# Performance work log

Hardware: AMD Instinct MI355X
Metric: run time of the kernel (lower is better)

## Reference

```python
import jax, jax.numpy as jnp
import numpy as np

N_NODES = 50000
N_EDGES = 800000
EMB = 128
HID = [128, 128]
OUT = 64
CE = 8  # stand-in for CROSS_ENTROPY_INDEXES: first 8 output columns get sigmoid


def _linear_params(key, d_in, d_out):
    k1, k2 = jax.random.split(key)
    s = 1.0 / np.sqrt(d_in)
    w = jax.random.uniform(k1, (d_in, d_out), minval=-s, maxval=s, dtype=jnp.float32)
    b = jax.random.uniform(k2, (d_out,), minval=-s, maxval=s, dtype=jnp.float32)
    return w, b


def setup_inputs() -> dict:
    key = jax.random.key(0)
    ks = jax.random.split(key, 16)
    z = jax.random.normal(ks[0], (N_NODES, EMB), dtype=jnp.float32)
    edge_index = jax.random.randint(ks[1], (2, N_EDGES), 0, N_NODES, dtype=jnp.int64)
    # SAGEConv params: neighbor weight (with bias) + root weight
    w1_n, b1 = _linear_params(ks[2], EMB, HID[0])
    w1_r, _ = _linear_params(ks[3], EMB, HID[0])
    w2_n, b2 = _linear_params(ks[4], HID[0], HID[1])
    w2_r, _ = _linear_params(ks[5], HID[0], HID[1])
    wf_n, bf = _linear_params(ks[6], HID[1], OUT)
    wf_r, _ = _linear_params(ks[7], HID[1], OUT)
    # initial residual linears: emb -> hid[1], emb -> out
    w_res1, b_res1 = _linear_params(ks[8], EMB, HID[1])
    w_res2, b_res2 = _linear_params(ks[9], EMB, OUT)
    return dict(z=z, edge_index=edge_index,
                w1_n=w1_n, w1_r=w1_r, b1=b1,
                w2_n=w2_n, w2_r=w2_r, b2=b2,
                wf_n=wf_n, wf_r=wf_r, bf=bf,
                w_res1=w_res1, b_res1=b_res1,
                w_res2=w_res2, b_res2=b_res2)


def _sage(x, src, dst, w_n, w_r, b, n_nodes):
    # mean-aggregate neighbor features at target nodes, then affine combine with root
    msg = x[src]                                        # [E, d]
    agg = jax.ops.segment_sum(msg, dst, num_segments=n_nodes)
    deg = jax.ops.segment_sum(jnp.ones_like(dst, dtype=x.dtype), dst, num_segments=n_nodes)
    mean = agg / jnp.maximum(deg, 1.0)[:, None]
    return mean @ w_n + x @ w_r + b


def reference(z, edge_index, w1_n, w1_r, b1, w2_n, w2_r, b2, wf_n, wf_r, bf,
              w_res1, b_res1, w_res2, b_res2):
    n = z.shape[0]
    src, dst = edge_index[0], edge_index[1]
    h = jax.nn.relu(_sage(z, src, dst, w1_n, w1_r, b1, n))
    # mid layer (dropout is identity in eval) + initial residual
    h = jax.nn.relu(_sage(h, src, dst, w2_n, w2_r, b2, n))
    h = h + (z @ w_res1 + b_res1)
    # final conv + final residual
    h = _sage(h, src, dst, wf_n, wf_r, bf, n)
    h = h + (z @ w_res2 + b_res2)
    # sigmoid on cross-entropy columns
    h = h.at[:, :CE].set(jax.nn.sigmoid(h[:, :CE]))
    return h
```

## Files before the change

### kernel.cpp

```cpp
#include <hip/hip_runtime.h>
#include <hip/hip_bf16.h>
#include <math.h>

#define NN 50000
#define NE 800000
#define NB 391
#define EPB 6250

typedef short bf16x8 __attribute__((ext_vector_type(8)));
typedef float f32x4 __attribute__((ext_vector_type(4)));
typedef unsigned short us4 __attribute__((ext_vector_type(4)));
typedef unsigned short us8 __attribute__((ext_vector_type(8)));
typedef unsigned int u32x4 __attribute__((ext_vector_type(4)));

__device__ __forceinline__ float bf2f(unsigned short u) {
  union { unsigned int i; float f; } x; x.i = ((unsigned int)u) << 16; return x.f;
}
__device__ __forceinline__ unsigned short f2bf(float f) {
  union { float f; unsigned int i; } x; x.f = f;
  unsigned int i = x.i;
  unsigned int r = i + 0x7FFF + ((i >> 16) & 1);
  return (unsigned short)(r >> 16);
}
__device__ __forceinline__ unsigned long long pk64(f32x4 v) {
  union { us4 s; unsigned long long u; } x;
  x.s[0] = f2bf(v[0]); x.s[1] = f2bf(v[1]); x.s[2] = f2bf(v[2]); x.s[3] = f2bf(v[3]);
  return x.u;
}
__device__ __forceinline__ us4 pack4(f32x4 v) {
  us4 o; o[0] = f2bf(v[0]); o[1] = f2bf(v[1]); o[2] = f2bf(v[2]); o[3] = f2bf(v[3]);
  return o;
}

__global__ __launch_bounds__(512) void bscan_kernel(const int* __restrict__ bhist,
                                                    int* __restrict__ bucket_off,
                                                    int* __restrict__ gcur) {
  __shared__ int s[512];
  int t = threadIdx.x;
  int v = (t < NB) ? bhist[t] : 0;
  s[t] = v; __syncthreads();
  for (int off = 1; off < 512; off <<= 1) {
    int x = (t >= off) ? s[t - off] : 0;
    __syncthreads();
    s[t] += x;
    __syncthreads();
  }
  if (t < NB) { bucket_off[t] = s[t] - v; gcur[t] = 0; }
  if (t == NB - 1) bucket_off[NB] = s[t];
}

__global__ __launch_bounds__(256) void bscat_kernel(const int* __restrict__ srcn,
                                                    const int* __restrict__ dstn,
                                                    const int* __restrict__ bucket_off,
                                                    int* __restrict__ gcur,
                                                    unsigned long long* __restrict__ ebuf) {
  __shared__ int hist[NB];
  __shared__ int base[NB];
  for (int i = threadIdx.x; i < NB; i += 256) hist[i] = 0;
  __syncthreads();
  int e0 = blockIdx.x * EPB;
  for (int i = threadIdx.x; i < EPB; i += 256)
    atomicAdd(&hist[dstn[e0 + i] >> 7], 1);
  __syncthreads();
  for (int i = threadIdx.x; i < NB; i += 256) {
    int c = hist[i];
    base[i] = c ? (bucket_off[i] + atomicAdd(&gcur[i], c)) : 0;
  }
  __syncthreads();
  for (int i = threadIdx.x; i < EPB; i += 256) {
    int s = srcn[e0 + i], d = dstn[e0 + i];
    int b = d >> 7;
    int pos = atomicSub(&hist[b], 1) - 1;
    ebuf[(size_t)base[b] + pos] = ((unsigned long long)(unsigned)d << 32) | (unsigned)s;
  }
}

__global__ __launch_bounds__(256) void bfill_kernel(const unsigned long long* __restrict__ ebuf,
                                                    const int* __restrict__ bucket_off,
                                                    int* __restrict__ rowoff,
                                                    int* __restrict__ csr) {
  int b = blockIdx.x;
  int bo = bucket_off[b], cnt = bucket_off[b + 1] - bo;
  __shared__ int ndeg[128], noff[128];
  int t = threadIdx.x;
  if (t < 128) ndeg[t] = 0;
  __syncthreads();
  for (int i = t; i < cnt; i += 256)
    atomicAdd(&ndeg[(int)(ebuf[bo + i] >> 32) & 127], 1);
  __syncthreads();
  if (t < 128) noff[t] = ndeg[t];
  __syncthreads();
  for (int off = 1; off < 128; off <<= 1) {
    int x = 0;
    if (t < 128 && t >= off) x = noff[t - off];
    __syncthreads();
    if (t < 128 && t >= off) noff[t] += x;
    __syncthreads();
  }
  if (t < 128) {
    int ex = noff[t] - ndeg[t];
    noff[t] = ex;
    int node = b * 128 + t;
    if (node < NN) rowoff[node] = bo + ex;
  }
  if (b == NB - 1 && t == 0) rowoff[NN] = NE;
  __syncthreads();
  for (int i = t; i < cnt; i += 256) {
    unsigned long long e = ebuf[bo + i];
    int dl = (int)(e >> 32) & 127;
    int pos = atomicSub(&ndeg[dl], 1) - 1;
    csr[bo + noff[dl] + pos] = (int)(unsigned)e;
  }
}

__global__ __launch_bounds__(256) void setup_kernel(
    const float* __restrict__ z, unsigned short* __restrict__ A1,
    const float* __restrict__ w1n, const float* __restrict__ w1r,
    const float* __restrict__ w2n, const float* __restrict__ w2r,
    const float* __restrict__ wfn, const float* __restrict__ wfr,
    const float* __restrict__ wr1, const float* __restrict__ wr2,
    unsigned short* __restrict__ Bp1, unsigned short* __restrict__ Bp2,
    unsigned short* __restrict__ Bp3,
    const int* __restrict__ dstn, int* __restrict__ bhist) {
  __shared__ int h[NB];
  int b = blockIdx.x;
  if (b < 6250) {
    int i = b * 256 + threadIdx.x;
    if (i >= NN * 128 / 4) return;
    int i4 = i * 4;
    int row = i4 >> 7, c = i4 & 127;
    f32x4 v = *(const f32x4*)(z + i4);
    us4 o = { f2bf(v[0]), f2bf(v[1]), f2bf(v[2]), f2bf(v[3]) };
    *(us4*)(A1 + (size_t)row * 256 + 128 + c) = o;
  } else if (b < 6314) {
    int g = (b - 6250) * 256 + threadIdx.x;
    unsigned short* D; int NT, fi;
    int which;
    if      (g < 10240) { fi = g;         D = Bp1; NT = 20; which = 1; }
    else if (g < 14336) { fi = g - 10240; D = Bp2; NT = 8;  which = 2; }
    else if (g < 16384) { fi = g - 14336; D = Bp3; NT = 4;  which = 3; }
    else return;
    int lane = fi & 63, t = fi >> 6;
    int nt = t % NT, k0i = t / NT;
    int m = lane & 15, q = lane >> 4;
    int kb = k0i * 32 + q * 8;
    int n = nt * 16 + m;
    int hi = (kb >= 128);
    int k0_ = kb - (hi ? 128 : 0);
    const float* W = nullptr; int Nseg = 128; int nn = n;
    if (which == 1) {
      if (n < 128)      { W = hi ? w1r : w1n; nn = n; Nseg = 128; }
      else if (n < 256) { W = hi ? wr1 : nullptr; nn = n - 128; Nseg = 128; }
      else              { W = hi ? wr2 : nullptr; nn = n - 256; Nseg = 64; }
    } else if (which == 2) { W = hi ? w2r : w2n; Nseg = 128; }
    else                   { W = hi ? wfr : wfn; Nseg = 64; }
    unsigned short o[8];
#pragma unroll
    for (int j = 0; j < 8; j++)
      o[j] = W ? f2bf(W[(size_t)(k0_ + j) * Nseg + nn]) : (unsigned short)0;
    *(us8*)(D + (size_t)fi * 8) = *(const us8*)o;
  } else {
    for (int i = threadIdx.x; i < NB; i += 256) h[i] = 0;
    __syncthreads();
    int e0 = (b - 6314) * EPB;
    for (int i = threadIdx.x; i < EPB; i += 256)
      atomicAdd(&h[dstn[e0 + i] >> 7], 1);
    __syncthreads();
    for (int i = threadIdx.x; i < NB; i += 256)
      if (h[i]) atomicAdd(&bhist[i], h[i]);
  }
}

__global__ __launch_bounds__(256) void agg_kernel(const unsigned short* __restrict__ feat, int fstride,
                                                  unsigned short* __restrict__ outm, int ostride,
                                                  const int* __restrict__ rowoff,
                                                  const int* __restrict__ csr) {
  int wave = threadIdx.x >> 6, lane = threadIdx.x & 63;
  int node = blockIdx.x * 4 + wave;
  if (node >= NN) return;
  int beg = rowoff[node], end = rowoff[node + 1];
  int g = lane >> 4;
  int c = (lane & 15) << 3;
  float a[8];
#pragma unroll
  for (int i = 0; i < 8; i++) a[i] = 0.f;
  int e1 = end - 1;
  for (int j = beg + g; j < end; j += 16) {
    int j1 = (j + 4 < e1) ? j + 4 : e1;
    int j2 = (j + 8 < e1) ? j + 8 : e1;
    int j3 = (j + 12 < e1) ? j + 12 : e1;
    int s0 = csr[j], s1 = csr[j1], s2 = csr[j2], s3 = csr[j3];
    float w1 = (j + 4 < end) ? 1.f : 0.f;
    float w2 = (j + 8 < end) ? 1.f : 0.f;
    float w3 = (j + 12 < end) ? 1.f : 0.f;
    u32x4 v0 = *(const u32x4*)(feat + (size_t)s0 * fstride + c);
    u32x4 v1 = *(const u32x4*)(feat + (size_t)s1 * fstride + c);
    u32x4 v2 = *(const u32x4*)(feat + (size_t)s2 * fstride + c);
    u32x4 v3 = *(const u32x4*)(feat + (size_t)s3 * fstride + c);
#pragma unroll
    for (int i = 0; i < 4; i++) {
      float l0 = bf2f((unsigned short)(v0[i] & 0xffff));
      float h0 = bf2f((unsigned short)(v0[i] >> 16));
      l0 = fmaf(w1, bf2f((unsigned short)(v1[i] & 0xffff)), l0);
      h0 = fmaf(w1, bf2f((unsigned short)(v1[i] >> 16)), h0);
      l0 = fmaf(w2, bf2f((unsigned short)(v2[i] & 0xffff)), l0);
      h0 = fmaf(w2, bf2f((unsigned short)(v2[i] >> 16)), h0);
      l0 = fmaf(w3, bf2f((unsigned short)(v3[i] & 0xffff)), l0);
      h0 = fmaf(w3, bf2f((unsigned short)(v3[i] >> 16)), h0);
      a[2*i] += l0;
      a[2*i+1] += h0;
    }
  }
#pragma unroll
  for (int i = 0; i < 8; i++) {
    a[i] += __shfl_xor(a[i], 16, 64);
    a[i] += __shfl_xor(a[i], 32, 64);
  }
  if (g == 0) {
    float inv = 1.f / fmaxf((float)(end - beg), 1.f);
    unsigned int o[4];
#pragma unroll
    for (int i = 0; i < 4; i++)
      o[i] = ((unsigned int)f2bf(a[2*i+1] * inv) << 16) | f2bf(a[2*i] * inv);
    *(u32x4*)(outm + (size_t)node * ostride + c) = *(const u32x4*)o;
  }
}

__global__ __launch_bounds__(256) void gemm1_kernel(
    const unsigned short* __restrict__ A,
    const unsigned short* __restrict__ Bp,
    const float* __restrict__ b1, const float* __restrict__ br1, const float* __restrict__ br2,
    unsigned short* __restrict__ h1out,
    unsigned short* __restrict__ res1, unsigned short* __restrict__ res2)
{
  const int NT = 20, TILES = 4;
  __shared__ unsigned short Bs[TILES * 8 * 512];
  int tid = threadIdx.x;
  int wave = tid >> 6, lane = tid & 63;
  int xg = blockIdx.x;
  int ybase = xg * TILES;
  int row0 = blockIdx.y * 128 + wave * 16;
  int m = lane & 15, q = lane >> 4;
  const float* bias; unsigned short* dst; int dstride, cbb; int relu;
  if (xg < 2)      { bias = b1 + xg * 64;        dst = h1out; dstride = 256; cbb = xg * 64;        relu = 1; }
  else if (xg < 4) { bias = br1 + (xg - 2) * 64; dst = res1;  dstride = 128; cbb = (xg - 2) * 64;  relu = 0; }
  else             { bias = br2;                 dst = res2;  dstride = 64;  cbb = 0;              relu = 0; }

  const unsigned short* arow0 = A + (size_t)(row0 + m) * 256 + q * 8;
  const unsigned short* arow1 = arow0 + 64 * 256;
  bf16x8 af0[8], af1[8];
#pragma unroll
  for (int k0i = 0; k0i < 8; ++k0i) {
    af0[k0i] = *(const bf16x8*)(arow0 + k0i * 32);
    af1[k0i] = *(const bf16x8*)(arow1 + k0i * 32);
  }
#pragma unroll
  for (int i = tid; i < TILES * 64 * 8; i += 256) {
    int k0i = i / (TILES * 64), r = i % (TILES * 64);
    *(us8*)(Bs + (size_t)k0i * TILES * 512 + (size_t)r * 8) =
        *(const us8*)(Bp + ((size_t)k0i * NT + ybase) * 512 + (size_t)r * 8);
  }
  __syncthreads();
  f32x4 acc[2][TILES];
#pragma unroll
  for (int h = 0; h < 2; h++)
#pragma unroll
    for (int i = 0; i < TILES; i++) acc[h][i] = (f32x4){0.f, 0.f, 0.f, 0.f};
#pragma unroll
  for (int k0i = 0; k0i < 8; ++k0i) {
    const unsigned short* bk = Bs + (size_t)k0i * TILES * 512 + lane * 8;
#pragma unroll
    for (int s = 0; s < TILES; ++s) {
      bf16x8 bfr = *(const bf16x8*)(bk + s * 512);
      acc[0][s] = __builtin_amdgcn_mfma_f32_16x16x32_bf16(bfr, af0[k0i], acc[0][s], 0, 0, 0);
      acc[1][s] = __builtin_amdgcn_mfma_f32_16x16x32_bf16(bfr, af1[k0i], acc[1][s], 0, 0, 0);
    }
  }
  int src0 = m + ((q & 1) ? 32 : 0);
#pragma unroll
  for (int h = 0; h < 2; h++) {
    int row = row0 + h * 64 + m;
#pragma unroll
    for (int p = 0; p < 2; p++) {
      f32x4 v0 = acc[h][2 * p], v1 = acc[h][2 * p + 1];
      f32x4 bb0 = *(const f32x4*)(bias + 32 * p + 4 * q);
      f32x4 bb1 = *(const f32x4*)(bias + 32 * p + 16 + 4 * q);
#pragma unroll
      for (int r = 0; r < 4; r++) { v0[r] += bb0[r]; v1[r] += bb1[r]; }
      if (relu) {
#pragma unroll
        for (int r = 0; r < 4; r++) { v0[r] = fmaxf(v0[r], 0.f); v1[r] = fmaxf(v1[r], 0.f); }
      }
      unsigned long long d0 = pk64(v0), d1 = pk64(v1);
      unsigned long long a0 = __shfl(d0, src0, 64);
      unsigned long long b0 = __shfl(d0, src0 + 16, 64);
      unsigned long long a1 = __shfl(d1, src0, 64);
      unsigned long long b1v = __shfl(d1, src0 + 16, 64);
      unsigned long long lo = (q >> 1) ? a1 : a0;
      unsigned long long hi = (q >> 1) ? b1v : b0;
      if (row < NN) {
        unsigned long long ov[2] = { lo, hi };
        *(us8*)(dst + (size_t)row * dstride + cbb + 32 * p + 8 * q) = *(const us8*)ov;
      }
    }
  }
}

__global__ __launch_bounds__(256) void gemm2_kernel(
    const unsigned short* __restrict__ A,
    const unsigned short* __restrict__ Bp,
    const float* __restrict__ b2,
    const unsigned short* __restrict__ res1,
    unsigned short* __restrict__ out_bf)
{
  const int NT = 8, TILES = 4;
  __shared__ unsigned short Bs[TILES * 8 * 512];
  int tid = threadIdx.x;
  int wave = tid >> 6, lane = tid & 63;
  int xg = blockIdx.x;
  int ybase = xg * TILES;
  int cbb = xg * 64;
  const float* bias = b2 + cbb;
  int row0 = blockIdx.y * 128 + wave * 16;
  int m = lane & 15, q = lane >> 4;
  const unsigned short* arow0 = A + (size_t)(row0 + m) * 256 + q * 8;
  const unsigned short* arow1 = arow0 + 64 * 256;
  bf16x8 af0[8], af1[8];
#pragma unroll
  for (int k0i = 0; k0i < 8; ++k0i) {
    af0[k0i] = *(const bf16x8*)(arow0 + k0i * 32);
    af1[k0i] = *(const bf16x8*)(arow1 + k0i * 32);
  }
#pragma unroll
  for (int i = tid; i < TILES * 64 * 8; i += 256) {
    int k0i = i / (TILES * 64), r = i % (TILES * 64);
    *(us8*)(Bs + (size_t)k0i * TILES * 512 + (size_t)r * 8) =
        *(const us8*)(Bp + ((size_t)k0i * NT + ybase) * 512 + (size_t)r * 8);
  }
  __syncthreads();
  f32x4 acc[2][TILES];
#pragma unroll
  for (int h = 0; h < 2; h++)
#pragma unroll
    for (int i = 0; i < TILES; i++) acc[h][i] = (f32x4){0.f, 0.f, 0.f, 0.f};
#pragma unroll
  for (int k0i = 0; k0i < 8; ++k0i) {
    const unsigned short* bk = Bs + (size_t)k0i * TILES * 512 + lane * 8;
#pragma unroll
    for (int s = 0; s < TILES; ++s) {
      bf16x8 bfr = *(const bf16x8*)(bk + s * 512);
      acc[0][s] = __builtin_amdgcn_mfma_f32_16x16x32_bf16(bfr, af0[k0i], acc[0][s], 0, 0, 0);
      acc[1][s] = __builtin_amdgcn_mfma_f32_16x16x32_bf16(bfr, af1[k0i], acc[1][s], 0, 0, 0);
    }
  }
  int src0 = m + ((q & 1) ? 32 : 0);
#pragma unroll
  for (int h = 0; h < 2; h++) {
    int row = row0 + h * 64 + m;
#pragma unroll
    for (int p = 0; p < 2; p++) {
      f32x4 v0 = acc[h][2 * p], v1 = acc[h][2 * p + 1];
      f32x4 bb0 = *(const f32x4*)(bias + 32 * p + 4 * q);
      f32x4 bb1 = *(const f32x4*)(bias + 32 * p + 16 + 4 * q);
#pragma unroll
      for (int r = 0; r < 4; r++) {
        v0[r] = fmaxf(v0[r] + bb0[r], 0.f);
        v1[r] = fmaxf(v1[r] + bb1[r], 0.f);
      }
      unsigned long long d0 = pk64(v0), d1 = pk64(v1);
      unsigned long long a0 = __shfl(d0, src0, 64);
      unsigned long long b0 = __shfl(d0, src0 + 16, 64);
      unsigned long long a1 = __shfl(d1, src0, 64);
      unsigned long long b1v = __shfl(d1, src0 + 16, 64);
      unsigned long long lo = (q >> 1) ? a1 : a0;
      unsigned long long hi = (q >> 1) ? b1v : b0;
      if (row < NN) {
        size_t off = cbb + 32 * p + 8 * q;
        us8 rv = *(const us8*)(res1 + (size_t)row * 128 + off);
        unsigned long long ov[2] = { lo, hi };
        unsigned short* e = (unsigned short*)ov;
#pragma unroll
        for (int r = 0; r < 8; r++) e[r] = f2bf(bf2f(e[r]) + bf2f(rv[r]));
        *(us8*)(out_bf + (size_t)row * 256 + off) = *(const us8*)ov;
      }
    }
  }
}

__global__ __launch_bounds__(256) void gemm3_kernel(
    const unsigned short* __restrict__ A,
    const unsigned short* __restrict__ Bp,
    const float* __restrict__ bias,
    const unsigned short* __restrict__ res2,
    float* __restrict__ out_f)
{
  const int NT = 4, TILES = 4;
  __shared__ unsigned short Bs[TILES * 8 * 512];
  int tid = threadIdx.x;
  int wave = tid >> 6, lane = tid & 63;
  int row0 = blockIdx.y * 64 + wave * 16;
  int m = lane & 15, q = lane >> 4;
  const unsigned short* arow = A + (size_t)(row0 + m) * 256 + q * 8;
  bf16x8 af[8];
#pragma unroll
  for (int k0i = 0; k0i < 8; ++k0i) af[k0i] = *(const bf16x8*)(arow + k0i * 32);
#pragma unroll
  for (int i = tid; i < TILES * 64 * 8; i += 256) {
    int k0i = i / (TILES * 64), r = i % (TILES * 64);
    *(us8*)(Bs + (size_t)k0i * TILES * 512 + (size_t)r * 8) =
        *(const us8*)(Bp + ((size_t)k0i * NT) * 512 + (size_t)r * 8);
  }
  __syncthreads();
  f32x4 acc[TILES];
#pragma unroll
  for (int i = 0; i < TILES; i++) acc[i] = (f32x4){0.f, 0.f, 0.f, 0.f};
#pragma unroll
  for (int k0i = 0; k0i < 8; ++k0i) {
    const unsigned short* bk = Bs + (size_t)k0i * TILES * 512 + lane * 8;
#pragma unroll
    for (int s = 0; s < TILES; ++s) {
      bf16x8 bfr = *(const bf16x8*)(bk + s * 512);
      acc[s] = __builtin_amdgcn_mfma_f32_16x16x32_bf16(bfr, af[k0i], acc[s], 0, 0, 0);
    }
  }
  int row = row0 + m;
  if (row >= NN) return;
  int cb = q * 4;
#pragma unroll
  for (int s = 0; s < TILES; ++s) {
    int col = s * 16 + cb;
    f32x4 v = acc[s];
    f32x4 bb = *(const f32x4*)(bias + col);
    us4 rv = *(const us4*)(res2 + (size_t)row * 64 + col);
#pragma unroll
    for (int r = 0; r < 4; r++) v[r] += bb[r] + bf2f(rv[r]);
    if (col < 8) {
#pragma unroll
      for (int r = 0; r < 4; r++) v[r] = 1.f / (1.f + __expf(-v[r]));
    }
    *(f32x4*)(out_f + (size_t)row * 64 + col) = v;
  }
}

extern "C" void kernel_launch(void* const* d_in, const int* in_sizes, int n_in,
                              void* d_out, int out_size, void* d_ws, size_t ws_size,
                              hipStream_t stream) {
  const float* z   = (const float*)d_in[0];
  const int*   edge = (const int*)d_in[1];
  const int*   srcn = edge;
  const int*   dstn = edge + NE;
  const float* w1n = (const float*)d_in[2];
  const float* w1r = (const float*)d_in[3];
  const float* b1  = (const float*)d_in[4];
  const float* w2n = (const float*)d_in[5];
  const float* w2r = (const float*)d_in[6];
  const float* b2  = (const float*)d_in[7];
  const float* wfn = (const float*)d_in[8];
  const float* wfr = (const float*)d_in[9];
  const float* bfb = (const float*)d_in[10];
  const float* wr1 = (const float*)d_in[11];
  const float* br1 = (const float*)d_in[12];
  const float* wr2 = (const float*)d_in[13];
  const float* br2 = (const float*)d_in[14];
  float* out = (float*)d_out;

  char* p = (char*)d_ws;
  auto alloc = [&](size_t bytes) { char* r = p; p += (bytes + 255) & ~255ull; return r; };
  int* rowoff = (int*)alloc((size_t)(NN + 1) * 4);
  int* bhist  = (int*)alloc((size_t)NB * 4);
  int* bucket_off = (int*)alloc((size_t)(NB + 1) * 4);
  int* gcur   = (int*)alloc((size_t)NB * 4);
  int* csr    = (int*)alloc((size_t)NE * 4);
  unsigned short* A1 = (unsigned short*)alloc((size_t)NN * 256 * 2);
  unsigned short* A2 = (unsigned short*)alloc((size_t)NN * 256 * 2);
  unsigned short* res1 = (unsigned short*)alloc((size_t)NN * 128 * 2);
  unsigned short* res2 = (unsigned short*)alloc((size_t)NN * 64 * 2);
  unsigned short* Bp1 = (unsigned short*)alloc(10240 * 8 * 2);
  unsigned short* Bp2 = (unsigned short*)alloc(4096 * 8 * 2);
  unsigned short* Bp3 = (unsigned short*)alloc(2048 * 8 * 2);
  unsigned short* A3 = A1;
  unsigned long long* ebuf = (unsigned long long*)res1;

  hipMemsetAsync(bhist, 0, (size_t)NB * 4, stream);
  setup_kernel<<<6442, 256, 0, stream>>>(z, A1, w1n, w1r, w2n, w2r, wfn, wfr, wr1, wr2,
                                         Bp1, Bp2, Bp3, dstn, bhist);
  bscan_kernel<<<1, 512, 0, stream>>>(bhist, bucket_off, gcur);
  bscat_kernel<<<128, 256, 0, stream>>>(srcn, dstn, bucket_off, gcur, ebuf);
  bfill_kernel<<<NB, 256, 0, stream>>>(ebuf, bucket_off, rowoff, csr);

  const int gy128 = (NN + 127) / 128;
  const int gy64  = (NN + 63) / 64;
  const int agg_blocks = (NN + 3) / 4;

  agg_kernel<<<agg_blocks, 256, 0, stream>>>(A1 + 128, 256, A1, 256, rowoff, csr);
  gemm1_kernel<<<dim3(5, gy128), 256, 0, stream>>>(A1, Bp1, b1, br1, br2, A2 + 128, res1, res2);

  agg_kernel<<<agg_blocks, 256, 0, stream>>>(A2 + 128, 256, A2, 256, rowoff, csr);
  gemm2_kernel<<<dim3(2, gy128), 256, 0, stream>>>(A2, Bp2, b2, res1, A3 + 128);

  agg_kernel<<<agg_blocks, 256, 0, stream>>>(A3 + 128, 256, A3, 256, rowoff, csr);
  gemm3_kernel<<<dim3(1, gy64), 256, 0, stream>>>(A3, Bp3, bfb, res2, out);
}
```

Measured before the change: 284.9 us.

## Fuse neighbor aggregation into per-layer GEMM kernels and merge bucket scan

Each SAGE layer's mean aggregation now runs inside its GEMM kernel: 512-thread blocks gather neighbor means for 128 rows into swizzled shared memory, then run MFMA against B tiles streamed per K-slice. This removes the intermediate mean buffer round-trip and three kernel launches. The standalone bucket-scan kernel is dropped; scatter and fill kernels recompute the prefix scan from the histogram, and feature buffers shrink to a 128-wide padded layout. The cost is only 391 blocks per layer, each with long serial gather loops, extra barriers per K-step, and redundant scans in every scatter/fill block.

```diff
diff --git a/kernel.cpp b/kernel.cpp
--- a/kernel.cpp
+++ b/kernel.cpp
@@ -3,6 +3,7 @@
 #include <math.h>
 
 #define NN 50000
+#define NNP 50048
 #define NE 800000
 #define NB 391
 #define EPB 6250
@@ -27,17 +28,9 @@
   x.s[0] = f2bf(v[0]); x.s[1] = f2bf(v[1]); x.s[2] = f2bf(v[2]); x.s[3] = f2bf(v[3]);
   return x.u;
 }
-__device__ __forceinline__ us4 pack4(f32x4 v) {
-  us4 o; o[0] = f2bf(v[0]); o[1] = f2bf(v[1]); o[2] = f2bf(v[2]); o[3] = f2bf(v[3]);
-  return o;
-}
-
-__global__ __launch_bounds__(512) void bscan_kernel(const int* __restrict__ bhist,
-                                                    int* __restrict__ bucket_off,
-                                                    int* __restrict__ gcur) {
-  __shared__ int s[512];
+
+__device__ __forceinline__ int scan_incl_512(int v, int* s) {
   int t = threadIdx.x;
-  int v = (t < NB) ? bhist[t] : 0;
   s[t] = v; __syncthreads();
   for (int off = 1; off < 512; off <<= 1) {
     int x = (t >= off) ? s[t - off] : 0;
@@ -45,29 +38,33 @@
     s[t] += x;
     __syncthreads();
   }
-  if (t < NB) { bucket_off[t] = s[t] - v; gcur[t] = 0; }
-  if (t == NB - 1) bucket_off[NB] = s[t];
-}
-
-__global__ __launch_bounds__(256) void bscat_kernel(const int* __restrict__ srcn,
+  return s[t];
+}
+
+__global__ __launch_bounds__(512) void bscat_kernel(const int* __restrict__ srcn,
                                                     const int* __restrict__ dstn,
-                                                    const int* __restrict__ bucket_off,
+                                                    const int* __restrict__ bhist,
                                                     int* __restrict__ gcur,
                                                     unsigned long long* __restrict__ ebuf) {
+  __shared__ int sbuf[512];
+  __shared__ int boff[NB];
   __shared__ int hist[NB];
   __shared__ int base[NB];
-  for (int i = threadIdx.x; i < NB; i += 256) hist[i] = 0;
+  int t = threadIdx.x;
+  int v = (t < NB) ? bhist[t] : 0;
+  int incl = scan_incl_512(v, sbuf);
+  if (t < NB) { boff[t] = incl - v; hist[t] = 0; }
   __syncthreads();
   int e0 = blockIdx.x * EPB;
-  for (int i = threadIdx.x; i < EPB; i += 256)
+  for (int i = t; i < EPB; i += 512)
     atomicAdd(&hist[dstn[e0 + i] >> 7], 1);
   __syncthreads();
-  for (int i = threadIdx.x; i < NB; i += 256) {
+  for (int i = t; i < NB; i += 512) {
     int c = hist[i];
-    base[i] = c ? (bucket_off[i] + atomicAdd(&gcur[i], c)) : 0;
-  }
-  __syncthreads();
-  for (int i = threadIdx.x; i < EPB; i += 256) {
+    base[i] = c ? (boff[i] + atomicAdd(&gcur[i], c)) : 0;
+  }
+  __syncthreads();
+  for (int i = t; i < EPB; i += 512) {
     int s = srcn[e0 + i], d = dstn[e0 + i];
     int b = d >> 7;
     int pos = atomicSub(&hist[b], 1) - 1;
@@ -75,17 +72,22 @@
   }
 }
 
-__global__ __launch_bounds__(256) void bfill_kernel(const unsigned long long* __restrict__ ebuf,
-                                                    const int* __restrict__ bucket_off,
+__global__ __launch_bounds__(512) void bfill_kernel(const unsigned long long* __restrict__ ebuf,
+                                                    const int* __restrict__ bhist,
                                                     int* __restrict__ rowoff,
                                                     int* __restrict__ csr) {
+  __shared__ int sbuf[512];
+  __shared__ int sb[2];
+  __shared__ int ndeg[128], noff[128];
   int b = blockIdx.x;
-  int bo = bucket_off[b], cnt = bucket_off[b + 1] - bo;
-  __shared__ int ndeg[128], noff[128];
   int t = threadIdx.x;
+  int v = (t < NB) ? bhist[t] : 0;
+  int incl = scan_incl_512(v, sbuf);
+  if (t == b) { sb[0] = incl - v; sb[1] = v; }
   if (t < 128) ndeg[t] = 0;
   __syncthreads();
-  for (int i = t; i < cnt; i += 256)
+  int bo = sb[0], cnt = sb[1];
+  for (int i = t; i < cnt; i += 512)
     atomicAdd(&ndeg[(int)(ebuf[bo + i] >> 32) & 127], 1);
   __syncthreads();
   if (t < 128) noff[t] = ndeg[t];
@@ -105,7 +107,7 @@
   }
   if (b == NB - 1 && t == 0) rowoff[NN] = NE;
   __syncthreads();
-  for (int i = t; i < cnt; i += 256) {
+  for (int i = t; i < cnt; i += 512) {
     unsigned long long e = ebuf[bo + i];
     int dl = (int)(e >> 32) & 127;
     int pos = atomicSub(&ndeg[dl], 1) - 1;
@@ -114,7 +116,7 @@
 }
 
 __global__ __launch_bounds__(256) void setup_kernel(
-    const float* __restrict__ z, unsigned short* __restrict__ A1,
+    const float* __restrict__ z, unsigned short* __restrict__ Z16,
     const float* __restrict__ w1n, const float* __restrict__ w1r,
     const float* __restrict__ w2n, const float* __restrict__ w2r,
     const float* __restrict__ wfn, const float* __restrict__ wfr,
@@ -131,7 +133,7 @@
     int row = i4 >> 7, c = i4 & 127;
     f32x4 v = *(const f32x4*)(z + i4);
     us4 o = { f2bf(v[0]), f2bf(v[1]), f2bf(v[2]), f2bf(v[3]) };
-    *(us4*)(A1 + (size_t)row * 256 + 128 + c) = o;
+    *(us4*)(Z16 + (size_t)row * 128 + c) = o;
   } else if (b < 6314) {
     int g = (b - 6250) * 256 + threadIdx.x;
     unsigned short* D; int NT, fi;
@@ -171,272 +173,280 @@
   }
 }
 
-__global__ __launch_bounds__(256) void agg_kernel(const unsigned short* __restrict__ feat, int fstride,
-                                                  unsigned short* __restrict__ outm, int ostride,
-                                                  const int* __restrict__ rowoff,
-                                                  const int* __restrict__ csr) {
-  int wave = threadIdx.x >> 6, lane = threadIdx.x & 63;
-  int node = blockIdx.x * 4 + wave;
-  if (node >= NN) return;
-  int beg = rowoff[node], end = rowoff[node + 1];
+__device__ __forceinline__ void gather_mean(const unsigned short* __restrict__ feat,
+                                            int row0,
+                                            const int* __restrict__ rowoff,
+                                            const int* __restrict__ csr,
+                                            unsigned short* meanS) {
+  int tid = threadIdx.x;
+  int w = tid >> 6, lane = tid & 63;
   int g = lane >> 4;
   int c = (lane & 15) << 3;
-  float a[8];
-#pragma unroll
-  for (int i = 0; i < 8; i++) a[i] = 0.f;
-  int e1 = end - 1;
-  for (int j = beg + g; j < end; j += 16) {
-    int j1 = (j + 4 < e1) ? j + 4 : e1;
-    int j2 = (j + 8 < e1) ? j + 8 : e1;
-    int j3 = (j + 12 < e1) ? j + 12 : e1;
-    int s0 = csr[j], s1 = csr[j1], s2 = csr[j2], s3 = csr[j3];
-    float w1 = (j + 4 < end) ? 1.f : 0.f;
-    float w2 = (j + 8 < end) ? 1.f : 0.f;
-    float w3 = (j + 12 < end) ? 1.f : 0.f;
-    u32x4 v0 = *(const u32x4*)(feat + (size_t)s0 * fstride + c);
-    u32x4 v1 = *(const u32x4*)(feat + (size_t)s1 * fstride + c);
-    u32x4 v2 = *(const u32x4*)(feat + (size_t)s2 * fstride + c);
-    u32x4 v3 = *(const u32x4*)(feat + (size_t)s3 * fstride + c);
-#pragma unroll
-    for (int i = 0; i < 4; i++) {
-      float l0 = bf2f((unsigned short)(v0[i] & 0xffff));
-      float h0 = bf2f((unsigned short)(v0[i] >> 16));
-      l0 = fmaf(w1, bf2f((unsigned short)(v1[i] & 0xffff)), l0);
-      h0 = fmaf(w1, bf2f((unsigned short)(v1[i] >> 16)), h0);
-      l0 = fmaf(w2, bf2f((unsigned short)(v2[i] & 0xffff)), l0);
-      h0 = fmaf(w2, bf2f((unsigned short)(v2[i] >> 16)), h0);
-      l0 = fmaf(w3, bf2f((unsigned short)(v3[i] & 0xffff)), l0);
-      h0 = fmaf(w3, bf2f((unsigned short)(v3[i] >> 16)), h0);
-      a[2*i] += l0;
-      a[2*i+1] += h0;
-    }
-  }
-#pragma unroll
-  for (int i = 0; i < 8; i++) {
-    a[i] += __shfl_xor(a[i], 16, 64);
-    a[i] += __shfl_xor(a[i], 32, 64);
-  }
-  if (g == 0) {
-    float inv = 1.f / fmaxf((float)(end - beg), 1.f);
-    unsigned int o[4];
-#pragma unroll
-    for (int i = 0; i < 4; i++)
-      o[i] = ((unsigned int)f2bf(a[2*i+1] * inv) << 16) | f2bf(a[2*i] * inv);
-    *(u32x4*)(outm + (size_t)node * ostride + c) = *(const u32x4*)o;
-  }
-}
-
-__global__ __launch_bounds__(256) void gemm1_kernel(
-    const unsigned short* __restrict__ A,
+#pragma unroll 2
+  for (int i = 0; i < 16; ++i) {
+    int node = row0 + w * 16 + i;
+    int beg = 0, end = 0;
+    if (node < NN) { beg = rowoff[node]; end = rowoff[node + 1]; }
+    float a[8];
+#pragma unroll
+    for (int k = 0; k < 8; ++k) a[k] = 0.f;
+    int e1 = end - 1;
+    for (int j = beg + g; j < end; j += 16) {
+      int j1 = (j + 4 < e1) ? j + 4 : e1;
+      int j2 = (j + 8 < e1) ? j + 8 : e1;
+      int j3 = (j + 12 < e1) ? j + 12 : e1;
+      int s0 = csr[j], s1 = csr[j1], s2 = csr[j2], s3 = csr[j3];
+      float w1 = (j + 4 < end) ? 1.f : 0.f;
+      float w2 = (j + 8 < end) ? 1.f : 0.f;
+      float w3 = (j + 12 < end) ? 1.f : 0.f;
+      u32x4 v0 = *(const u32x4*)(feat + (size_t)s0 * 128 + c);
+      u32x4 v1 = *(const u32x4*)(feat + (size_t)s1 * 128 + c);
+      u32x4 v2 = *(const u32x4*)(feat + (size_t)s2 * 128 + c);
+      u32x4 v3 = *(const u32x4*)(feat + (size_t)s3 * 128 + c);
+#pragma unroll
+      for (int k = 0; k < 4; ++k) {
+        float l0 = bf2f((unsigned short)(v0[k] & 0xffff));
+        float h0 = bf2f((unsigned short)(v0[k] >> 16));
+        l0 = fmaf(w1, bf2f((unsigned short)(v1[k] & 0xffff)), l0);
+        h0 = fmaf(w1, bf2f((unsigned short)(v1[k] >> 16)), h0);
+        l0 = fmaf(w2, bf2f((unsigned short)(v2[k] & 0xffff)), l0);
+        h0 = fmaf(w2, bf2f((unsigned short)(v2[k] >> 16)), h0);
+        l0 = fmaf(w3, bf2f((unsigned short)(v3[k] & 0xffff)), l0);
+        h0 = fmaf(w3, bf2f((unsigned short)(v3[k] >> 16)), h0);
+        a[2 * k] += l0;
+        a[2 * k + 1] += h0;
+      }
+    }
+#pragma unroll
+    for (int k = 0; k < 8; ++k) {
+      a[k] += __shfl_xor(a[k], 16, 64);
+      a[k] += __shfl_xor(a[k], 32, 64);
+    }
+    if (g == 0) {
+      float inv = 1.f / fmaxf((float)(end - beg), 1.f);
+      unsigned int o[4];
+#pragma unroll
+      for (int k = 0; k < 4; ++k)
+        o[k] = ((unsigned int)f2bf(a[2 * k + 1] * inv) << 16) | f2bf(a[2 * k] * inv);
+      int rl = w * 16 + i;
+      int byte = rl * 256 + (c << 1);
+      byte ^= ((i & 7) << 4);
+      *(u32x4*)((char*)meanS + byte) = *(const u32x4*)o;
+    }
+  }
+}
+
+__device__ __forceinline__ bf16x8 mean_frag(const unsigned short* meanS,
+                                            int w, int m, int q, int k0i) {
+  int rl = w * 16 + m;
+  int byte = rl * 256 + q * 16 + k0i * 64;
+  byte ^= ((m & 7) << 4);
+  return *(const bf16x8*)((const char*)meanS + byte);
+}
+
+__device__ __forceinline__ void stage_B(unsigned short* Bs, const unsigned short* __restrict__ Bp,
+                                        int k0i, int T, int NTfull, int tid) {
+  for (int i = tid; i < T * 64; i += 512) {
+    int t = i >> 6, r = i & 63;
+    *(us8*)(Bs + (size_t)t * 512 + (size_t)r * 8) =
+        *(const us8*)(Bp + ((size_t)(k0i * NTfull + t)) * 512 + (size_t)r * 8);
+  }
+}
+
+__global__ __launch_bounds__(512, 4) void fused1_kernel(
+    const unsigned short* __restrict__ Z16,
     const unsigned short* __restrict__ Bp,
     const float* __restrict__ b1, const float* __restrict__ br1, const float* __restrict__ br2,
-    unsigned short* __restrict__ h1out,
-    unsigned short* __restrict__ res1, unsigned short* __restrict__ res2)
+    const int* __restrict__ rowoff, const int* __restrict__ csr,
+    unsigned short* __restrict__ h1, unsigned short* __restrict__ res1,
+    unsigned short* __restrict__ res2)
 {
-  const int NT = 20, TILES = 4;
-  __shared__ unsigned short Bs[TILES * 8 * 512];
+  __shared__ unsigned short meanS[128 * 128];
+  __shared__ unsigned short Bs[20 * 512];
   int tid = threadIdx.x;
-  int wave = tid >> 6, lane = tid & 63;
-  int xg = blockIdx.x;
-  int ybase = xg * TILES;
-  int row0 = blockIdx.y * 128 + wave * 16;
+  int w = tid >> 6, lane = tid & 63;
   int m = lane & 15, q = lane >> 4;
-  const float* bias; unsigned short* dst; int dstride, cbb; int relu;
-  if (xg < 2)      { bias = b1 + xg * 64;        dst = h1out; dstride = 256; cbb = xg * 64;        relu = 1; }
-  else if (xg < 4) { bias = br1 + (xg - 2) * 64; dst = res1;  dstride = 128; cbb = (xg - 2) * 64;  relu = 0; }
-  else             { bias = br2;                 dst = res2;  dstride = 64;  cbb = 0;              relu = 0; }
-
-  const unsigned short* arow0 = A + (size_t)(row0 + m) * 256 + q * 8;
-  const unsigned short* arow1 = arow0 + 64 * 256;
-  bf16x8 af0[8], af1[8];
+  int row0 = blockIdx.x * 128;
+  int row = row0 + w * 16 + m;
+  bf16x8 afx[4];
+  const unsigned short* xr = Z16 + (size_t)row * 128 + q * 8;
+#pragma unroll
+  for (int k = 0; k < 4; ++k) afx[k] = *(const bf16x8*)(xr + k * 32);
+  stage_B(Bs, Bp, 0, 8, 20, tid);
+  gather_mean(Z16, row0, rowoff, csr, meanS);
+  __syncthreads();
+  f32x4 acc[20];
+#pragma unroll
+  for (int t = 0; t < 20; ++t) acc[t] = (f32x4){0.f, 0.f, 0.f, 0.f};
 #pragma unroll
   for (int k0i = 0; k0i < 8; ++k0i) {
-    af0[k0i] = *(const bf16x8*)(arow0 + k0i * 32);
-    af1[k0i] = *(const bf16x8*)(arow1 + k0i * 32);
-  }
-#pragma unroll
-  for (int i = tid; i < TILES * 64 * 8; i += 256) {
-    int k0i = i / (TILES * 64), r = i % (TILES * 64);
-    *(us8*)(Bs + (size_t)k0i * TILES * 512 + (size_t)r * 8) =
-        *(const us8*)(Bp + ((size_t)k0i * NT + ybase) * 512 + (size_t)r * 8);
-  }
-  __syncthreads();
-  f32x4 acc[2][TILES];
-#pragma unroll
-  for (int h = 0; h < 2; h++)
-#pragma unroll
-    for (int i = 0; i < TILES; i++) acc[h][i] = (f32x4){0.f, 0.f, 0.f, 0.f};
-#pragma unroll
-  for (int k0i = 0; k0i < 8; ++k0i) {
-    const unsigned short* bk = Bs + (size_t)k0i * TILES * 512 + lane * 8;
-#pragma unroll
-    for (int s = 0; s < TILES; ++s) {
-      bf16x8 bfr = *(const bf16x8*)(bk + s * 512);
-      acc[0][s] = __builtin_amdgcn_mfma_f32_16x16x32_bf16(bfr, af0[k0i], acc[0][s], 0, 0, 0);
-      acc[1][s] = __builtin_amdgcn_mfma_f32_16x16x32_bf16(bfr, af1[k0i], acc[1][s], 0, 0, 0);
+    const unsigned short* bk = Bs + lane * 8;
+    if (k0i < 4) {
+      bf16x8 af = mean_frag(meanS, w, m, q, k0i);
+#pragma unroll
+      for (int t = 0; t < 8; ++t)
+        acc[t] = __builtin_amdgcn_mfma_f32_16x16x32_bf16(*(const bf16x8*)(bk + t * 512), af, acc[t], 0, 0, 0);
+    } else {
+      bf16x8 af = afx[k0i - 4];
+#pragma unroll
+      for (int t = 0; t < 20; ++t)
+        acc[t] = __builtin_amdgcn_mfma_f32_16x16x32_bf16(*(const bf16x8*)(bk + t * 512), af, acc[t], 0, 0, 0);
+    }
+    __syncthreads();
+    if (k0i < 7) {
+      stage_B(Bs, Bp, k0i + 1, (k0i + 1 < 4) ? 8 : 20, 20, tid);
+      __syncthreads();
     }
   }
   int src0 = m + ((q & 1) ? 32 : 0);
 #pragma unroll
-  for (int h = 0; h < 2; h++) {
-    int row = row0 + h * 64 + m;
-#pragma unroll
-    for (int p = 0; p < 2; p++) {
-      f32x4 v0 = acc[h][2 * p], v1 = acc[h][2 * p + 1];
-      f32x4 bb0 = *(const f32x4*)(bias + 32 * p + 4 * q);
-      f32x4 bb1 = *(const f32x4*)(bias + 32 * p + 16 + 4 * q);
-#pragma unroll
-      for (int r = 0; r < 4; r++) { v0[r] += bb0[r]; v1[r] += bb1[r]; }
-      if (relu) {
-#pragma unroll
-        for (int r = 0; r < 4; r++) { v0[r] = fmaxf(v0[r], 0.f); v1[r] = fmaxf(v1[r], 0.f); }
-      }
-      unsigned long long d0 = pk64(v0), d1 = pk64(v1);
-      unsigned long long a0 = __shfl(d0, src0, 64);
-      unsigned long long b0 = __shfl(d0, src0 + 16, 64);
-      unsigned long long a1 = __shfl(d1, src0, 64);
-      unsigned long long b1v = __shfl(d1, src0 + 16, 64);
-      unsigned long long lo = (q >> 1) ? a1 : a0;
-      unsigned long long hi = (q >> 1) ? b1v : b0;
-      if (row < NN) {
-        unsigned long long ov[2] = { lo, hi };
-        *(us8*)(dst + (size_t)row * dstride + cbb + 32 * p + 8 * q) = *(const us8*)ov;
-      }
-    }
-  }
-}
-
-__global__ __launch_bounds__(256) void gemm2_kernel(
-    const unsigned short* __restrict__ A,
+  for (int p = 0; p < 10; ++p) {
+    const float* bias; unsigned short* dst; int dstride, colb, relu;
+    if (p < 4)      { bias = b1  + 32 * p;       dst = h1;   dstride = 128; colb = 32 * p;       relu = 1; }
+    else if (p < 8) { bias = br1 + 32 * (p - 4); dst = res1; dstride = 128; colb = 32 * (p - 4); relu = 0; }
+    else            { bias = br2 + 32 * (p - 8); dst = res2; dstride = 64;  colb = 32 * (p - 8); relu = 0; }
+    f32x4 v0 = acc[2 * p], v1 = acc[2 * p + 1];
+    f32x4 bb0 = *(const f32x4*)(bias + 4 * q);
+    f32x4 bb1 = *(const f32x4*)(bias + 16 + 4 * q);
+#pragma unroll
+    for (int r = 0; r < 4; ++r) { v0[r] += bb0[r]; v1[r] += bb1[r]; }
+    if (relu) {
+#pragma unroll
+      for (int r = 0; r < 4; ++r) { v0[r] = fmaxf(v0[r], 0.f); v1[r] = fmaxf(v1[r], 0.f); }
+    }
+    unsigned long long d0 = pk64(v0), d1 = pk64(v1);
+    unsigned long long a0 = __shfl(d0, src0, 64);
+    unsigned long long b0 = __shfl(d0, src0 + 16, 64);
+    unsigned long long a1 = __shfl(d1, src0, 64);
+    unsigned long long b1v = __shfl(d1, src0 + 16, 64);
+    unsigned long long lo = (q >> 1) ? a1 : a0;
+    unsigned long long hi = (q >> 1) ? b1v : b0;
+    if (row < NN) {
+      unsigned long long ov[2] = { lo, hi };
+      *(us8*)(dst + (size_t)row * dstride + colb + 8 * q) = *(const us8*)ov;
+    }
+  }
+}
+
+__global__ __launch_bounds__(512, 4) void fused2_kernel(
+    const unsigned short* __restrict__ H1,
     const unsigned short* __restrict__ Bp,
     const float* __restrict__ b2,
+    const int* __restrict__ rowoff, const int* __restrict__ csr,
     const unsigned short* __restrict__ res1,
-    unsigned short* __restrict__ out_bf)
+    unsigned short* __restrict__ h2)
 {
-  const int NT = 8, TILES = 4;
-  __shared__ unsigned short Bs[TILES * 8 * 512];
+  __shared__ unsigned short meanS[128 * 128];
+  __shared__ unsigned short Bs[8 * 512];
   int tid = threadIdx.x;
-  int wave = tid >> 6, lane = tid & 63;
-  int xg = blockIdx.x;
-  int ybase = xg * TILES;
-  int cbb = xg * 64;
-  const float* bias = b2 + cbb;
-  int row0 = blockIdx.y * 128 + wave * 16;
+  int w = tid >> 6, lane = tid & 63;
   int m = lane & 15, q = lane >> 4;
-  const unsigned short* arow0 = A + (size_t)(row0 + m) * 256 + q * 8;
-  const unsigned short* arow1 = arow0 + 64 * 256;
-  bf16x8 af0[8], af1[8];
+  int row0 = blockIdx.x * 128;
+  int row = row0 + w * 16 + m;
+  bf16x8 afx[4];
+  const unsigned short* xr = H1 + (size_t)row * 128 + q * 8;
+#pragma unroll
+  for (int k = 0; k < 4; ++k) afx[k] = *(const bf16x8*)(xr + k * 32);
+  stage_B(Bs, Bp, 0, 8, 8, tid);
+  gather_mean(H1, row0, rowoff, csr, meanS);
+  __syncthreads();
+  f32x4 acc[8];
+#pragma unroll
+  for (int t = 0; t < 8; ++t) acc[t] = (f32x4){0.f, 0.f, 0.f, 0.f};
 #pragma unroll
   for (int k0i = 0; k0i < 8; ++k0i) {
-    af0[k0i] = *(const bf16x8*)(arow0 + k0i * 32);
-    af1[k0i] = *(const bf16x8*)(arow1 + k0i * 32);
-  }
-#pragma unroll
-  for (int i = tid; i < TILES * 64 * 8; i += 256) {
-    int k0i = i / (TILES * 64), r = i % (TILES * 64);
-    *(us8*)(Bs + (size_t)k0i * TILES * 512 + (size_t)r * 8) =
-        *(const us8*)(Bp + ((size_t)k0i * NT + ybase) * 512 + (size_t)r * 8);
-  }
-  __syncthreads();
-  f32x4 acc[2][TILES];
-#pragma unroll
-  for (int h = 0; h < 2; h++)
-#pragma unroll
-    for (int i = 0; i < TILES; i++) acc[h][i] = (f32x4){0.f, 0.f, 0.f, 0.f};
-#pragma unroll
-  for (int k0i = 0; k0i < 8; ++k0i) {
-    const unsigned short* bk = Bs + (size_t)k0i * TILES * 512 + lane * 8;
-#pragma unroll
-    for (int s = 0; s < TILES; ++s) {
-      bf16x8 bfr = *(const bf16x8*)(bk + s * 512);
-      acc[0][s] = __builtin_amdgcn_mfma_f32_16x16x32_bf16(bfr, af0[k0i], acc[0][s], 0, 0, 0);
-      acc[1][s] = __builtin_amdgcn_mfma_f32_16x16x32_bf16(bfr, af1[k0i], acc[1][s], 0, 0, 0);
+    const unsigned short* bk = Bs + lane * 8;
+    bf16x8 af = (k0i < 4) ? mean_frag(meanS, w, m, q, k0i) : afx[k0i - 4];
+#pragma unroll
+    for (int t = 0; t < 8; ++t)
+      acc[t] = __builtin_amdgcn_mfma_f32_16x16x32_bf16(*(const bf16x8*)(bk + t * 512), af, acc[t], 0, 0, 0);
+    __syncthreads();
+    if (k0i < 7) {
+      stage_B(Bs, Bp, k0i + 1, 8, 8, tid);
+      __syncthreads();
     }
   }
   int src0 = m + ((q & 1) ? 32 : 0);
 #pragma unroll
-  for (int h = 0; h < 2; h++) {
-    int row = row0 + h * 64 + m;
-#pragma unroll
-    for (int p = 0; p < 2; p++) {
-      f32x4 v0 = acc[h][2 * p], v1 = acc[h][2 * p + 1];
-      f32x4 bb0 = *(const f32x4*)(bias + 32 * p + 4 * q);
-      f32x4 bb1 = *(const f32x4*)(bias + 32 * p + 16 + 4 * q);
-#pragma unroll
-      for (int r = 0; r < 4; r++) {
-        v0[r] = fmaxf(v0[r] + bb0[r], 0.f);
-        v1[r] = fmaxf(v1[r] + bb1[r], 0.f);
-      }
-      unsigned long long d0 = pk64(v0), d1 = pk64(v1);
-      unsigned long long a0 = __shfl(d0, src0, 64);
-      unsigned long long b0 = __shfl(d0, src0 + 16, 64);
-      unsigned long long a1 = __shfl(d1, src0, 64);
-      unsigned long long b1v = __shfl(d1, src0 + 16, 64);
-      unsigned long long lo = (q >> 1) ? a1 : a0;
-      unsigned long long hi = (q >> 1) ? b1v : b0;
-      if (row < NN) {
-        size_t off = cbb + 32 * p + 8 * q;
-        us8 rv = *(const us8*)(res1 + (size_t)row * 128 + off);
-        unsigned long long ov[2] = { lo, hi };
-        unsigned short* e = (unsigned short*)ov;
-#pragma unroll
-        for (int r = 0; r < 8; r++) e[r] = f2bf(bf2f(e[r]) + bf2f(rv[r]));
-        *(us8*)(out_bf + (size_t)row * 256 + off) = *(const us8*)ov;
-      }
-    }
-  }
-}
-
-__global__ __launch_bounds__(256) void gemm3_kernel(
-    const unsigned short* __restrict__ A,
+  for (int p = 0; p < 4; ++p) {
+    f32x4 v0 = acc[2 * p], v1 = acc[2 * p + 1];
+    f32x4 bb0 = *(const f32x4*)(b2 + 32 * p + 4 * q);
+    f32x4 bb1 = *(const f32x4*)(b2 + 32 * p + 16 + 4 * q);
+#pragma unroll
+    for (int r = 0; r < 4; ++r) {
+      v0[r] = fmaxf(v0[r] + bb0[r], 0.f);
+      v1[r] = fmaxf(v1[r] + bb1[r], 0.f);
+    }
+    unsigned long long d0 = pk64(v0), d1 = pk64(v1);
+    unsigned long long a0 = __shfl(d0, src0, 64);
+    unsigned long long b0 = __shfl(d0, src0 + 16, 64);
+    unsigned long long a1 = __shfl(d1, src0, 64);
+    unsigned long long b1v = __shfl(d1, src0 + 16, 64);
+    unsigned long long lo = (q >> 1) ? a1 : a0;
+    unsigned long long hi = (q >> 1) ? b1v : b0;
+    if (row < NN) {
+      size_t off = 32 * p + 8 * q;
+      us8 rv = *(const us8*)(res1 + (size_t)row * 128 + off);
+      unsigned long long ov[2] = { lo, hi };
+      unsigned short* e = (unsigned short*)ov;
+#pragma unroll
+      for (int r = 0; r < 8; ++r) e[r] = f2bf(bf2f(e[r]) + bf2f(rv[r]));
+      *(us8*)(h2 + (size_t)row * 128 + off) = *(const us8*)ov;
+    }
+  }
+}
+
+__global__ __launch_bounds__(512, 4) void fused3_kernel(
+    const unsigned short* __restrict__ H2,
     const unsigned short* __restrict__ Bp,
     const float* __restrict__ bias,
+    const int* __restrict__ rowoff, const int* __restrict__ csr,
     const unsigned short* __restrict__ res2,
     float* __restrict__ out_f)
 {
-  const int NT = 4, TILES = 4;
-  __shared__ unsigned short Bs[TILES * 8 * 512];
+  __shared__ unsigned short meanS[128 * 128];
+  __shared__ unsigned short Bs[4 * 512];
   int tid = threadIdx.x;
-  int wave = tid >> 6, lane = tid & 63;
-  int row0 = blockIdx.y * 64 + wave * 16;
+  int w = tid >> 6, lane = tid & 63;
   int m = lane & 15, q = lane >> 4;
-  const unsigned short* arow = A + (size_t)(row0 + m) * 256 + q * 8;
-  bf16x8 af[8];
-#pragma unroll
-  for (int k0i = 0; k0i < 8; ++k0i) af[k0i] = *(const bf16x8*)(arow + k0i * 32);
-#pragma unroll
-  for (int i = tid; i < TILES * 64 * 8; i += 256) {
-    int k0i = i / (TILES * 64), r = i % (TILES * 64);
-    *(us8*)(Bs + (size_t)k0i * TILES * 512 + (size_t)r * 8) =
-        *(const us8*)(Bp + ((size_t)k0i * NT) * 512 + (size_t)r * 8);
-  }
-  __syncthreads();
-  f32x4 acc[TILES];
-#pragma unroll
-  for (int i = 0; i < TILES; i++) acc[i] = (f32x4){0.f, 0.f, 0.f, 0.f};
+  int row0 = blockIdx.x * 128;
+  int row = row0 + w * 16 + m;
+  bf16x8 afx[4];
+  const unsigned short* xr = H2 + (size_t)row * 128 + q * 8;
+#pragma unroll
+  for (int k = 0; k < 4; ++k) afx[k] = *(const bf16x8*)(xr + k * 32);
+  stage_B(Bs, Bp, 0, 4, 4, tid);
+  gather_mean(H2, row0, rowoff, csr, meanS);
+  __syncthreads();
+  f32x4 acc[4];
+#pragma unroll
+  for (int t = 0; t < 4; ++t) acc[t] = (f32x4){0.f, 0.f, 0.f, 0.f};
 #pragma unroll
   for (int k0i = 0; k0i < 8; ++k0i) {
-    const unsigned short* bk = Bs + (size_t)k0i * TILES * 512 + lane * 8;
-#pragma unroll
-    for (int s = 0; s < TILES; ++s) {
-      bf16x8 bfr = *(const bf16x8*)(bk + s * 512);
-      acc[s] = __builtin_amdgcn_mfma_f32_16x16x32_bf16(bfr, af[k0i], acc[s], 0, 0, 0);
-    }
-  }
-  int row = row0 + m;
+    const unsigned short* bk = Bs + lane * 8;
+    bf16x8 af = (k0i < 4) ? mean_frag(meanS, w, m, q, k0i) : afx[k0i - 4];
+#pragma unroll
+    for (int t = 0; t < 4; ++t)
+      acc[t] = __builtin_amdgcn_mfma_f32_16x16x32_bf16(*(const bf16x8*)(bk + t * 512), af, acc[t], 0, 0, 0);
+    __syncthreads();
+    if (k0i < 7) {
+      stage_B(Bs, Bp, k0i + 1, 4, 4, tid);
+      __syncthreads();
+    }
+  }
   if (row >= NN) return;
   int cb = q * 4;
 #pragma unroll
-  for (int s = 0; s < TILES; ++s) {
+  for (int s = 0; s < 4; ++s) {
     int col = s * 16 + cb;
     f32x4 v = acc[s];
     f32x4 bb = *(const f32x4*)(bias + col);
     us4 rv = *(const us4*)(res2 + (size_t)row * 64 + col);
 #pragma unroll
-    for (int r = 0; r < 4; r++) v[r] += bb[r] + bf2f(rv[r]);
+    for (int r = 0; r < 4; ++r) v[r] += bb[r] + bf2f(rv[r]);
     if (col < 8) {
 #pragma unroll
-      for (int r = 0; r < 4; r++) v[r] = 1.f / (1.f + __expf(-v[r]));
+      for (int r = 0; r < 4; ++r) v[r] = 1.f / (1.f + __expf(-v[r]));
     }
     *(f32x4*)(out_f + (size_t)row * 64 + col) = v;
   }
@@ -467,37 +477,28 @@
   char* p = (char*)d_ws;
   auto alloc = [&](size_t bytes) { char* r = p; p += (bytes + 255) & ~255ull; return r; };
   int* rowoff = (int*)alloc((size_t)(NN + 1) * 4);
-  int* bhist  = (int*)alloc((size_t)NB * 4);
-  int* bucket_off = (int*)alloc((size_t)(NB + 1) * 4);
-  int* gcur   = (int*)alloc((size_t)NB * 4);
+  int* bhist  = (int*)alloc((size_t)2 * NB * 4);
+  int* gcur   = bhist + NB;
   int* csr    = (int*)alloc((size_t)NE * 4);
-  unsigned short* A1 = (unsigned short*)alloc((size_t)NN * 256 * 2);
-  unsigned short* A2 = (unsigned short*)alloc((size_t)NN * 256 * 2);
+  unsigned short* Z16 = (unsigned short*)alloc((size_t)NNP * 128 * 2);
+  unsigned short* H1  = (unsigned short*)alloc((size_t)NNP * 128 * 2);
+  unsigned short* H2  = (unsigned short*)alloc((size_t)NNP * 128 * 2);
   unsigned short* res1 = (unsigned short*)alloc((size_t)NN * 128 * 2);
   unsigned short* res2 = (unsigned short*)alloc((size_t)NN * 64 * 2);
   unsigned short* Bp1 = (unsigned short*)alloc(10240 * 8 * 2);
   unsigned short* Bp2 = (unsigned short*)alloc(4096 * 8 * 2);
   unsigned short* Bp3 = (unsigned short*)alloc(2048 * 8 * 2);
-  unsigned short* A3 = A1;
   unsigned long long* ebuf = (unsigned long long*)res1;
 
-  hipMemsetAsync(bhist, 0, (size_t)NB * 4, stream);
-  setup_kernel<<<6442, 256, 0, stream>>>(z, A1, w1n, w1r, w2n, w2r, wfn, wfr, wr1, wr2,
+  hipMemsetAsync(bhist, 0, (size_t)2 * NB * 4, stream);
+  setup_kernel<<<6442, 256, 0, stream>>>(z, Z16, w1n, w1r, w2n, w2r, wfn, wfr, wr1, wr2,
                                          Bp1, Bp2, Bp3, dstn, bhist);
-  bscan_kernel<<<1, 512, 0, stream>>>(bhist, bucket_off, gcur);
-  bscat_kernel<<<128, 256, 0, stream>>>(srcn, dstn, bucket_off, gcur, ebuf);
-  bfill_kernel<<<NB, 256, 0, stream>>>(ebuf, bucket_off, rowoff, csr);
-
-  const int gy128 = (NN + 127) / 128;
-  const int gy64  = (NN + 63) / 64;
-  const int agg_blocks = (NN + 3) / 4;
-
-  agg_kernel<<<agg_blocks, 256, 0, stream>>>(A1 + 128, 256, A1, 256, rowoff, csr);
-  gemm1_kernel<<<dim3(5, gy128), 256, 0, stream>>>(A1, Bp1, b1, br1, br2, A2 + 128, res1, res2);
-
-  agg_kernel<<<agg_blocks, 256, 0, stream>>>(A2 + 128, 256, A2, 256, rowoff, csr);
-  gemm2_kernel<<<dim3(2, gy128), 256, 0, stream>>>(A2, Bp2, b2, res1, A3 + 128);
-
-  agg_kernel<<<agg_blocks, 256, 0, stream>>>(A3 + 128, 256, A3, 256, rowoff, csr);
-  gemm3_kernel<<<dim3(1, gy64), 256, 0, stream>>>(A3, Bp3, bfb, res2, out);
-}
+  bscat_kernel<<<128, 512, 0, stream>>>(srcn, dstn, bhist, gcur, ebuf);
+  bfill_kernel<<<NB, 512, 0, stream>>>(ebuf, bhist, rowoff, csr);
+
+  const int gy = NNP / 128;
+
+  fused1_kernel<<<gy, 512, 0, stream>>>(Z16, Bp1, b1, br1, br2, rowoff, csr, H1, res1, res2);
+  fused2_kernel<<<gy, 512, 0, stream>>>(H1, Bp2, b2, rowoff, csr, res1, H2);
+  fused3_kernel<<<gy, 512, 0, stream>>>(H2, Bp3, bfb, rowoff, csr, res2, out);
+}
```

After: 296.1 us. 3.9% more time.
